# Kernel optimization log

Hardware: AMD Instinct MI355X
Metric: run time of the kernel (lower is better)

Reference implementation:

```python
import jax, jax.numpy as jnp
import numpy as np

N_NODES = 50000
N_EDGES = 800000
X_DIM = 32
E_DIM = 32
HID = 64
OUT = 32


def setup_inputs() -> dict:
    key = jax.random.key(0)
    ks = jax.random.split(key, 6)
    x = jax.random.normal(ks[0], (N_NODES, X_DIM), dtype=jnp.float32)
    edge_index = jax.random.randint(ks[1], (2, N_EDGES), 0, N_NODES, dtype=jnp.int64)
    edge_attr = jax.random.normal(ks[2], (N_EDGES, E_DIM), dtype=jnp.float32)
    in_dim = 2 * X_DIM + E_DIM  # 96
    W1 = jax.random.normal(ks[3], (in_dim, HID), dtype=jnp.float32) * (1.0 / np.sqrt(in_dim))
    b1 = jnp.zeros((HID,), dtype=jnp.float32)
    W2 = jax.random.normal(ks[4], (HID, OUT), dtype=jnp.float32) * (1.0 / np.sqrt(HID))
    b2 = jnp.zeros((OUT,), dtype=jnp.float32)
    return {"x": x, "edge_index": edge_index, "edge_attr": edge_attr,
            "W1": W1, "b1": b1, "W2": W2, "b2": b2}


def reference(x, edge_index, edge_attr, W1, b1, W2, b2):
    num_nodes = x.shape[0]
    rol, col = edge_index[0], edge_index[1]
    # gather endpoint features + edge attr -> [E, 2*x_dim + e_dim]
    e_feat = jnp.concatenate([x[rol], x[col], edge_attr], axis=-1)
    # 2-layer MLP (ReLU hidden)
    h = jax.nn.relu(e_feat @ W1 + b1)
    v = h @ W2 + b2  # [E, OUT]
    # scatter-max aggregation into destination nodes (empty segments -> -inf)
    x_cand = jax.ops.segment_max(v, col, num_segments=num_nodes)
    # elementwise max residual against trailing slice of x
    return jnp.maximum(x_cand, x[:, -v.shape[-1]:])
```

## Files before the change

kernel.cpp:

```cpp
#include <hip/hip_runtime.h>


constexpr int XD   = 32;
constexpr int HID  = 64;
constexpr int OUTD = 32;
constexpr int BM   = 128;
constexpr int ASTR = 104;
constexpr int HSTR = 72;
constexpr int BIN_SHIFT = 5;
constexpr int BINW  = 1 << BIN_SHIFT;
constexpr int BLK_E = 8192;
constexpr int EPB   = BLK_E / 256;

typedef __attribute__((ext_vector_type(8)))  short    short8;
typedef __attribute__((ext_vector_type(4)))  float    f32x4;
typedef __attribute__((ext_vector_type(4)))  float    floatx4;

static __device__ __forceinline__ unsigned f2bf(float f) {
    union { float f; unsigned u; } x; x.f = f;
    unsigned r = x.u + 0x7fff + ((x.u >> 16) & 1);
    return r >> 16;
}
static __device__ __forceinline__ unsigned encf(float f) {
    unsigned u = __float_as_uint(f);
    return (u >> 31) ? ~u : (u | 0x80000000u);
}
static __device__ __forceinline__ float decf(unsigned k) {
    return __uint_as_float((k >> 31) ? (k & 0x7fffffffu) : ~k);
}

__global__ __launch_bounds__(256) void prep_hist(
    const float* __restrict__ x, unsigned* __restrict__ xbf,
    const float* __restrict__ W1, const float* __restrict__ W2,
    unsigned* __restrict__ w1s, unsigned* __restrict__ w2s,
    const int* __restrict__ ei, unsigned* __restrict__ cnt,
    int n_edges, int nbins, int nblk, int total8)
{
    __shared__ unsigned lh[2048];
    const int t = threadIdx.x;
    const int b = blockIdx.x;

    if (b < nblk) {
        for (int i = t; i < nbins; i += 256) lh[i] = 0u;
        __syncthreads();
        const int chunk = b * BLK_E;
#pragma unroll
        for (int i = 0; i < EPB; ++i) {
            const int e = chunk + i * 256 + t;
            if (e < n_edges)
                atomicAdd(&lh[((unsigned)ei[n_edges + e]) >> BIN_SHIFT], 1u);
        }
        __syncthreads();
        for (int i = t; i < nbins; i += 256)
            cnt[(size_t)b * nbins + i] = lh[i];
        return;
    }

    const int i = (b - nblk) * 256 + t;

    if (i < total8) {
        const float4* src = reinterpret_cast<const float4*>(x) + (size_t)i * 2;
        float4 a = src[0], bb = src[1];
        uint4 o;
        o.x = f2bf(a.x)  | (f2bf(a.y)  << 16);
        o.y = f2bf(a.z)  | (f2bf(a.w)  << 16);
        o.z = f2bf(bb.x) | (f2bf(bb.y) << 16);
        o.w = f2bf(bb.z) | (f2bf(bb.w) << 16);
        reinterpret_cast<uint4*>(xbf)[i] = o;
    }

    if (i < 768) {
        const int ti = i >> 6, lane = i & 63;
        const int nt = ti / 3, ks = ti % 3;
        const int col = nt * 16 + (lane & 15);
        const int k0  = ks * 32 + ((lane >> 4) << 3);
        unsigned o[4];
#pragma unroll
        for (int p = 0; p < 4; ++p)
            o[p] = f2bf(W1[(k0 + 2 * p) * HID + col]) |
                   (f2bf(W1[(k0 + 2 * p + 1) * HID + col]) << 16);
        reinterpret_cast<uint4*>(w1s)[i] = make_uint4(o[0], o[1], o[2], o[3]);
    } else if (i < 1024) {
        const int tt = i - 768;
        const int ti = tt >> 6, lane = tt & 63;
        const int nt = ti >> 1, ks = ti & 1;
        const int col = nt * 16 + (lane & 15);
        const int k0  = ks * 32 + ((lane >> 4) << 3);
        unsigned o[4];
#pragma unroll
        for (int p = 0; p < 4; ++p)
            o[p] = f2bf(W2[(k0 + 2 * p) * OUTD + col]) |
                   (f2bf(W2[(k0 + 2 * p + 1) * OUTD + col]) << 16);
        reinterpret_cast<uint4*>(w2s)[tt] = make_uint4(o[0], o[1], o[2], o[3]);
    }
}

__global__ __launch_bounds__(128) void bin_off(
    const unsigned* __restrict__ cnt, unsigned* __restrict__ off,
    unsigned* __restrict__ totals, int nblk, int nbins)
{
    __shared__ unsigned ts[128];
    const int j = blockIdx.x;
    const int t = threadIdx.x;
    const unsigned d = (t < nblk) ? cnt[(size_t)t * nbins + j] : 0u;
    ts[t] = d;
    __syncthreads();
#pragma unroll
    for (int o = 1; o < 128; o <<= 1) {
        unsigned v = (t >= o) ? ts[t - o] : 0u;
        __syncthreads();
        ts[t] += v;
        __syncthreads();
    }
    if (t < nblk) off[(size_t)t * nbins + j] = ts[t] - d;
    if (t == 127) totals[j] = ts[127];
}

__global__ __launch_bounds__(256) void base_scan(
    const unsigned* __restrict__ totals, unsigned* __restrict__ base, int nbins)
{
    __shared__ unsigned ts[256];
    const int t = threadIdx.x;
    unsigned d[8];
    unsigned s = 0;
#pragma unroll
    for (int k = 0; k < 8; ++k) {
        const int i = t * 8 + k;
        d[k] = (i < nbins) ? totals[i] : 0u;
        s += d[k];
    }
    ts[t] = s;
    __syncthreads();
#pragma unroll
    for (int o = 1; o < 256; o <<= 1) {
        unsigned v = (t >= o) ? ts[t - o] : 0u;
        __syncthreads();
        ts[t] += v;
        __syncthreads();
    }
    unsigned run = (t == 0) ? 0u : ts[t - 1];
#pragma unroll
    for (int k = 0; k < 8; ++k) {
        const int i = t * 8 + k;
        if (i < nbins) base[i] = run;
        run += d[k];
    }
    if (t == 255) base[nbins] = run;
}

__global__ __launch_bounds__(256) void bin_write(
    const int* __restrict__ ei, const unsigned* __restrict__ off,
    const unsigned* __restrict__ base, uint2* __restrict__ rec,
    int n_edges, int nbins)
{
    __shared__ unsigned loff[2048];
    __shared__ unsigned lrank[2048];
    const int t = threadIdx.x;
    const int b = blockIdx.x;
    for (int i = t; i < nbins; i += 256) {
        loff[i]  = base[i] + off[(size_t)b * nbins + i];
        lrank[i] = 0u;
    }
    __syncthreads();
    const int chunk = b * BLK_E;
#pragma unroll
    for (int i = 0; i < EPB; ++i) {
        const int e = chunk + i * 256 + t;
        if (e < n_edges) {
            const unsigned row = (unsigned)ei[e];
            const unsigned col = (unsigned)ei[n_edges + e];
            const unsigned bin = col >> BIN_SHIFT;
            const unsigned r   = atomicAdd(&lrank[bin], 1u);
            rec[loff[bin] + r] = make_uint2((row << 16) | col, (unsigned)e);
        }
    }
}

__global__ __launch_bounds__(256) void edge_mlp_fused(
    const unsigned* __restrict__ xbf,
    const uint2*    __restrict__ rec,
    const float*    __restrict__ ea,
    const unsigned* __restrict__ w1s,
    const unsigned* __restrict__ w2s,
    const float*    __restrict__ b1,
    const float*    __restrict__ b2,
    const float*    __restrict__ x,
    const unsigned* __restrict__ base,
    float*          __restrict__ out,
    int n_edges, int n_nodes)
{
    __shared__ alignas(16) unsigned short S[BM * ASTR];
    __shared__ unsigned accK[BINW * OUTD];
    __shared__ unsigned rcsE[BM];
    __shared__ unsigned rcsR[BM];
    __shared__ unsigned rcsC[BM];

    const int t    = threadIdx.x;
    const int lane = t & 63;
    const int wave = t >> 6;
    const int bin  = blockIdx.x;
    const int n0   = bin << BIN_SHIFT;

    const unsigned sbeg = base[bin];
    const unsigned send = base[bin + 1];

    short8 w1f[12];
#pragma unroll
    for (int ti = 0; ti < 12; ++ti)
        w1f[ti] = *reinterpret_cast<const short8*>(w1s + (size_t)(ti * 64 + lane) * 4);
    short8 w2f[4];
#pragma unroll
    for (int ti = 0; ti < 4; ++ti)
        w2f[ti] = *reinterpret_cast<const short8*>(w2s + (size_t)(ti * 64 + lane) * 4);
    float bb1[4];
#pragma unroll
    for (int nt = 0; nt < 4; ++nt) bb1[nt] = b1[nt * 16 + (lane & 15)];
    float bb2[2];
#pragma unroll
    for (int nt = 0; nt < 2; ++nt) bb2[nt] = b2[nt * 16 + (lane & 15)];

#pragma unroll
    for (int k = 0; k < (BINW * OUTD) / 256; ++k) {
        const int idx = t + k * 256;
        const int g   = n0 + (idx >> 5);
        const float r = (g < n_nodes) ? x[(size_t)g * XD + (idx & 31)] : 0.0f;
        accK[idx] = encf(r);
    }

    const int ntile = (int)(send - sbeg + BM - 1) / BM;
    for (int tile = 0; tile < ntile; ++tile) {
        __syncthreads();

        if (t < BM) {
            unsigned p = sbeg + tile * BM + t;
            if (p >= send) p = send - 1;
            const uint2 q = rec[p];
            rcsE[t] = q.y; rcsR[t] = q.x >> 16; rcsC[t] = q.x & 0xffffu;
        }
        __syncthreads();

        {
            const int m    = t & 127;
            const int side = t >> 7;
            const unsigned id = side ? rcsC[m] : rcsR[m];
            const uint4* src = reinterpret_cast<const uint4*>(xbf + (size_t)id * 16);
#pragma unroll
            for (int q = 0; q < 4; ++q)
                *reinterpret_cast<uint4*>(&S[m * ASTR + side * 32 + q * 8]) = src[q];
        }
        {
#pragma unroll
            for (int i = 0; i < 4; ++i) {
                const int f = t + i * 256;
                const int m = f >> 3;
                const int c = (f & 7) * 4;
                const unsigned e = rcsE[m];
                const floatx4 d = __builtin_nontemporal_load(
                    reinterpret_cast<const floatx4*>(ea + (size_t)e * 32 + c));
                uint2 pk;
                pk.x = f2bf(d.x) | (f2bf(d.y) << 16);
                pk.y = f2bf(d.z) | (f2bf(d.w) << 16);
                *reinterpret_cast<uint2*>(&S[m * ASTR + 64 + c]) = pk;
            }
        }
        __syncthreads();

        f32x4 acc1[2][4];
#pragma unroll
        for (int mi = 0; mi < 2; ++mi)
#pragma unroll
            for (int nt = 0; nt < 4; ++nt) acc1[mi][nt] = (f32x4){0.f, 0.f, 0.f, 0.f};
#pragma unroll
        for (int ks = 0; ks < 3; ++ks) {
#pragma unroll
            for (int mi = 0; mi < 2; ++mi) {
                const int mt = wave * 2 + mi;
                short8 afrag = *reinterpret_cast<const short8*>(
                    &S[(mt * 16 + (lane & 15)) * ASTR + ks * 32 + ((lane >> 4) << 3)]);
#pragma unroll
                for (int nt = 0; nt < 4; ++nt)
                    acc1[mi][nt] = __builtin_amdgcn_mfma_f32_16x16x32_bf16(
                        afrag, w1f[nt * 3 + ks], acc1[mi][nt], 0, 0, 0);
            }
        }
        __syncthreads();

#pragma unroll
        for (int mi = 0; mi < 2; ++mi) {
            const int mt = wave * 2 + mi;
#pragma unroll
            for (int nt = 0; nt < 4; ++nt)
#pragma unroll
                for (int r = 0; r < 4; ++r) {
                    const float h = fmaxf(acc1[mi][nt][r] + bb1[nt], 0.0f);
                    S[(mt * 16 + ((lane >> 4) << 2) + r) * HSTR + nt * 16 + (lane & 15)] =
                        (unsigned short)f2bf(h);
                }
        }

        f32x4 acc2[2][2];
#pragma unroll
        for (int mi = 0; mi < 2; ++mi)
#pragma unroll
            for (int nt = 0; nt < 2; ++nt) acc2[mi][nt] = (f32x4){0.f, 0.f, 0.f, 0.f};
#pragma unroll
        for (int ks = 0; ks < 2; ++ks) {
#pragma unroll
            for (int mi = 0; mi < 2; ++mi) {
                const int mt = wave * 2 + mi;
                short8 hfrag = *reinterpret_cast<const short8*>(
                    &S[(mt * 16 + (lane & 15)) * HSTR + ks * 32 + ((lane >> 4) << 3)]);
#pragma unroll
                for (int nt = 0; nt < 2; ++nt)
                    acc2[mi][nt] = __builtin_amdgcn_mfma_f32_16x16x32_bf16(
                        hfrag, w2f[nt * 2 + ks], acc2[mi][nt], 0, 0, 0);
            }
        }

#pragma unroll
        for (int mi = 0; mi < 2; ++mi) {
            const int mt = wave * 2 + mi;
#pragma unroll
            for (int nt = 0; nt < 2; ++nt)
#pragma unroll
                for (int r = 0; r < 4; ++r) {
                    const int row = mt * 16 + ((lane >> 4) << 2) + r;
                    const float val = acc2[mi][nt][r] + bb2[nt];
                    const int ln = (int)rcsC[row] - n0;
                    atomicMax(&accK[ln * OUTD + nt * 16 + (lane & 15)], encf(val));
                }
        }
    }

    __syncthreads();
#pragma unroll
    for (int k = 0; k < (BINW * OUTD) / 256; ++k) {
        const int idx = t + k * 256;
        const int g   = n0 + (idx >> 5);
        if (g < n_nodes)
            out[(size_t)g * OUTD + (idx & 31)] = decf(accK[idx]);
    }
}

extern "C" void kernel_launch(void* const* d_in, const int* in_sizes, int n_in,
                              void* d_out, int out_size, void* d_ws, size_t ws_size,
                              hipStream_t stream)
{
    const float* x  = (const float*)d_in[0];
    const int*   ei = (const int*)  d_in[1];
    const float* ea = (const float*)d_in[2];
    const float* W1 = (const float*)d_in[3];
    const float* b1 = (const float*)d_in[4];
    const float* W2 = (const float*)d_in[5];
    const float* b2 = (const float*)d_in[6];
    float* out = (float*)d_out;

    const int n_nodes = in_sizes[0] / XD;
    const int n_edges = in_sizes[2] / 32;
    const int nbins   = (n_nodes + BINW - 1) >> BIN_SHIFT;
    const int nblk    = (n_edges + BLK_E - 1) / BLK_E;

    size_t off_b = 0;
    unsigned* cnt    = (unsigned*)((char*)d_ws + off_b); off_b += (size_t)nblk * nbins * 4;
    unsigned* offm   = (unsigned*)((char*)d_ws + off_b); off_b += (size_t)nblk * nbins * 4;
    unsigned* totals = (unsigned*)((char*)d_ws + off_b); off_b += (size_t)nbins * 4;
    unsigned* basep  = (unsigned*)((char*)d_ws + off_b); off_b += (size_t)(nbins + 1) * 4;
    off_b = (off_b + 15) & ~(size_t)15;
    uint2*    rec    = (uint2*)   ((char*)d_ws + off_b); off_b += (size_t)n_edges * 8;
    unsigned* xbf    = (unsigned*)((char*)d_ws + off_b); off_b += (size_t)n_nodes * 16 * 4;
    unsigned* w1s    = (unsigned*)((char*)d_ws + off_b); off_b += 768 * 16;
    unsigned* w2s    = (unsigned*)((char*)d_ws + off_b);

    const int total8     = n_nodes * XD / 8;
    const int prep_blk   = (max(total8, 1024) + 255) / 256;

    prep_hist<<<nblk + prep_blk, 256, 0, stream>>>(
        x, xbf, W1, W2, w1s, w2s, ei, cnt, n_edges, nbins, nblk, total8);
    bin_off<<<nbins, 128, 0, stream>>>(cnt, offm, totals, nblk, nbins);
    base_scan<<<1, 256, 0, stream>>>(totals, basep, nbins);
    bin_write<<<nblk, 256, 0, stream>>>(ei, offm, basep, rec, n_edges, nbins);
    edge_mlp_fused<<<nbins, 256, 0, stream>>>(
        xbf, rec, ea, w1s, w2s, b1, b2, x, basep, out, n_edges, n_nodes);
}
```

Measured before the change: 98.57 us.

## Prefetch next tile's edge records and edge attributes into registers

Edge record indices are now held in per-thread registers instead of shared arrays, which removes one barrier per tile. The next tile's record and its edge_attr row half are loaded into registers before the current tile's MFMA work, so global latency overlaps compute. Each thread now loads a contiguous 64-byte half of one edge's attributes instead of strided chunks. In exchange, register pressure rises from the prefetched float4s, which could lower occupancy.

Result: slower. 128.6 us (+30.5%).

```diff
diff --git a/kernel.cpp b/kernel.cpp
--- a/kernel.cpp
+++ b/kernel.cpp
@@ -191,8 +191,6 @@
 {
     __shared__ alignas(16) unsigned short S[BM * ASTR];
     __shared__ unsigned accK[BINW * OUTD];
-    __shared__ unsigned rcsE[BM];
-    __shared__ unsigned rcsR[BM];
     __shared__ unsigned rcsC[BM];
 
     const int t    = threadIdx.x;
@@ -201,6 +199,9 @@
     const int bin  = blockIdx.x;
     const int n0   = bin << BIN_SHIFT;
 
+    const int m    = t & 127;
+    const int side = t >> 7;
+
     const unsigned sbeg = base[bin];
     const unsigned send = base[bin + 1];
 
@@ -228,42 +229,60 @@
     }
 
     const int ntile = (int)(send - sbeg + BM - 1) / BM;
+
+    unsigned myE = 0, myR = 0, myC = 0;
+    floatx4  eg[4];
+
+    if (ntile > 0) {
+        unsigned p = sbeg + (unsigned)m;
+        if (p >= send) p = send - 1;
+        const uint2 q = rec[p];
+        myE = q.y; myR = q.x >> 16; myC = q.x & 0xffffu;
+        const floatx4* es = reinterpret_cast<const floatx4*>(
+            ea + (size_t)myE * 32 + side * 16);
+#pragma unroll
+        for (int k = 0; k < 4; ++k) eg[k] = __builtin_nontemporal_load(es + k);
+    }
+
     for (int tile = 0; tile < ntile; ++tile) {
-        __syncthreads();
-
-        if (t < BM) {
-            unsigned p = sbeg + tile * BM + t;
+        unsigned nE = myE, nR = myR, nC = myC;
+        if (tile + 1 < ntile) {
+            unsigned p = sbeg + (unsigned)(tile + 1) * BM + m;
             if (p >= send) p = send - 1;
             const uint2 q = rec[p];
-            rcsE[t] = q.y; rcsR[t] = q.x >> 16; rcsC[t] = q.x & 0xffffu;
-        }
+            nE = q.y; nR = q.x >> 16; nC = q.x & 0xffffu;
+        }
+
         __syncthreads();
 
         {
-            const int m    = t & 127;
-            const int side = t >> 7;
-            const unsigned id = side ? rcsC[m] : rcsR[m];
-            const uint4* src = reinterpret_cast<const uint4*>(xbf + (size_t)id * 16);
-#pragma unroll
-            for (int q = 0; q < 4; ++q)
-                *reinterpret_cast<uint4*>(&S[m * ASTR + side * 32 + q * 8]) = src[q];
-        }
-        {
-#pragma unroll
-            for (int i = 0; i < 4; ++i) {
-                const int f = t + i * 256;
-                const int m = f >> 3;
-                const int c = (f & 7) * 4;
-                const unsigned e = rcsE[m];
-                const floatx4 d = __builtin_nontemporal_load(
-                    reinterpret_cast<const floatx4*>(ea + (size_t)e * 32 + c));
+            const unsigned gid = side ? myC : myR;
+            const uint4* src = reinterpret_cast<const uint4*>(xbf + (size_t)gid * 16);
+            uint4 xg0 = src[0], xg1 = src[1], xg2 = src[2], xg3 = src[3];
+
+#pragma unroll
+            for (int k = 0; k < 4; ++k) {
                 uint2 pk;
-                pk.x = f2bf(d.x) | (f2bf(d.y) << 16);
-                pk.y = f2bf(d.z) | (f2bf(d.w) << 16);
-                *reinterpret_cast<uint2*>(&S[m * ASTR + 64 + c]) = pk;
+                pk.x = f2bf(eg[k].x) | (f2bf(eg[k].y) << 16);
+                pk.y = f2bf(eg[k].z) | (f2bf(eg[k].w) << 16);
+                *reinterpret_cast<uint2*>(&S[m * ASTR + 64 + side * 16 + k * 4]) = pk;
             }
-        }
-        __syncthreads();
+            if (side == 0) rcsC[m] = myC;
+
+            *reinterpret_cast<uint4*>(&S[m * ASTR + side * 32 +  0]) = xg0;
+            *reinterpret_cast<uint4*>(&S[m * ASTR + side * 32 +  8]) = xg1;
+            *reinterpret_cast<uint4*>(&S[m * ASTR + side * 32 + 16]) = xg2;
+            *reinterpret_cast<uint4*>(&S[m * ASTR + side * 32 + 24]) = xg3;
+        }
+        __syncthreads();
+
+        myE = nE; myR = nR; myC = nC;
+        if (tile + 1 < ntile) {
+            const floatx4* es = reinterpret_cast<const floatx4*>(
+                ea + (size_t)myE * 32 + side * 16);
+#pragma unroll
+            for (int k = 0; k < 4; ++k) eg[k] = __builtin_nontemporal_load(es + k);
+        }
 
         f32x4 acc1[2][4];
 #pragma unroll
```

## Load MFMA A-fragments directly from global memory instead of staging through LDS

Applied to the files above, without the earlier changes.

The first-layer input tile is no longer staged in shared memory. Each lane now gathers its own bf16 node-feature fragments and edge-attribute fragments from global memory straight into MFMA operand registers. This drops the LDS staging writes, the fragment reads and two block barriers per tile, and shrinks the LDS footprint, which may raise occupancy. In exchange the global loads are less coalesced: 16-byte per-lane gathers replace the cooperative row copies, the edge_attr loads lose the nontemporal hint, and each wave waits on its own loads before the MFMAs.

Result: faster. 92.21 us (-6.5%).

```diff
diff --git a/kernel.cpp b/kernel.cpp
--- a/kernel.cpp
+++ b/kernel.cpp
@@ -5,7 +5,6 @@
 constexpr int HID  = 64;
 constexpr int OUTD = 32;
 constexpr int BM   = 128;
-constexpr int ASTR = 104;
 constexpr int HSTR = 72;
 constexpr int BIN_SHIFT = 5;
 constexpr int BINW  = 1 << BIN_SHIFT;
@@ -189,7 +188,7 @@
     float*          __restrict__ out,
     int n_edges, int n_nodes)
 {
-    __shared__ alignas(16) unsigned short S[BM * ASTR];
+    __shared__ alignas(16) unsigned short Hlds[BM * HSTR];
     __shared__ unsigned accK[BINW * OUTD];
     __shared__ unsigned rcsE[BM];
     __shared__ unsigned rcsR[BM];
@@ -228,62 +227,55 @@
     }
 
     const int ntile = (int)(send - sbeg + BM - 1) / BM;
+    const int koff  = lane >> 4;
+
     for (int tile = 0; tile < ntile; ++tile) {
         __syncthreads();
 
         if (t < BM) {
-            unsigned p = sbeg + tile * BM + t;
+            unsigned p = sbeg + (unsigned)tile * BM + t;
             if (p >= send) p = send - 1;
             const uint2 q = rec[p];
             rcsE[t] = q.y; rcsR[t] = q.x >> 16; rcsC[t] = q.x & 0xffffu;
         }
         __syncthreads();
 
-        {
-            const int m    = t & 127;
-            const int side = t >> 7;
-            const unsigned id = side ? rcsC[m] : rcsR[m];
-            const uint4* src = reinterpret_cast<const uint4*>(xbf + (size_t)id * 16);
-#pragma unroll
-            for (int q = 0; q < 4; ++q)
-                *reinterpret_cast<uint4*>(&S[m * ASTR + side * 32 + q * 8]) = src[q];
-        }
-        {
-#pragma unroll
-            for (int i = 0; i < 4; ++i) {
-                const int f = t + i * 256;
-                const int m = f >> 3;
-                const int c = (f & 7) * 4;
-                const unsigned e = rcsE[m];
-                const floatx4 d = __builtin_nontemporal_load(
-                    reinterpret_cast<const floatx4*>(ea + (size_t)e * 32 + c));
-                uint2 pk;
-                pk.x = f2bf(d.x) | (f2bf(d.y) << 16);
-                pk.y = f2bf(d.z) | (f2bf(d.w) << 16);
-                *reinterpret_cast<uint2*>(&S[m * ASTR + 64 + c]) = pk;
+        f32x4 acc1[2][4];
+#pragma unroll
+        for (int mi = 0; mi < 2; ++mi)
+#pragma unroll
+            for (int nt = 0; nt < 4; ++nt) acc1[mi][nt] = (f32x4){0.f, 0.f, 0.f, 0.f};
+
+#pragma unroll
+        for (int mi = 0; mi < 2; ++mi) {
+            const int row16 = (wave * 2 + mi) * 16 + (lane & 15);
+            const unsigned idR = rcsR[row16];
+            const unsigned idC = rcsC[row16];
+            const unsigned eid = rcsE[row16];
+
+            const short8 aR = *reinterpret_cast<const short8*>(
+                xbf + (size_t)idR * 16 + koff * 4);
+            const short8 aC = *reinterpret_cast<const short8*>(
+                xbf + (size_t)idC * 16 + koff * 4);
+            const floatx4* ep = reinterpret_cast<const floatx4*>(
+                ea + (size_t)eid * 32 + koff * 8);
+            const floatx4 e0 = ep[0], e1 = ep[1];
+            union { uint4 u; short8 s; } ae;
+            ae.u.x = f2bf(e0.x) | (f2bf(e0.y) << 16);
+            ae.u.y = f2bf(e0.z) | (f2bf(e0.w) << 16);
+            ae.u.z = f2bf(e1.x) | (f2bf(e1.y) << 16);
+            ae.u.w = f2bf(e1.z) | (f2bf(e1.w) << 16);
+
+#pragma unroll
+            for (int nt = 0; nt < 4; ++nt) {
+                acc1[mi][nt] = __builtin_amdgcn_mfma_f32_16x16x32_bf16(
+                    aR, w1f[nt * 3 + 0], acc1[mi][nt], 0, 0, 0);
+                acc1[mi][nt] = __builtin_amdgcn_mfma_f32_16x16x32_bf16(
+                    aC, w1f[nt * 3 + 1], acc1[mi][nt], 0, 0, 0);
+                acc1[mi][nt] = __builtin_amdgcn_mfma_f32_16x16x32_bf16(
+                    ae.s, w1f[nt * 3 + 2], acc1[mi][nt], 0, 0, 0);
             }
         }
-        __syncthreads();
-
-        f32x4 acc1[2][4];
-#pragma unroll
-        for (int mi = 0; mi < 2; ++mi)
-#pragma unroll
-            for (int nt = 0; nt < 4; ++nt) acc1[mi][nt] = (f32x4){0.f, 0.f, 0.f, 0.f};
-#pragma unroll
-        for (int ks = 0; ks < 3; ++ks) {
-#pragma unroll
-            for (int mi = 0; mi < 2; ++mi) {
-                const int mt = wave * 2 + mi;
-                short8 afrag = *reinterpret_cast<const short8*>(
-                    &S[(mt * 16 + (lane & 15)) * ASTR + ks * 32 + ((lane >> 4) << 3)]);
-#pragma unroll
-                for (int nt = 0; nt < 4; ++nt)
-                    acc1[mi][nt] = __builtin_amdgcn_mfma_f32_16x16x32_bf16(
-                        afrag, w1f[nt * 3 + ks], acc1[mi][nt], 0, 0, 0);
-            }
-        }
-        __syncthreads();
 
 #pragma unroll
         for (int mi = 0; mi < 2; ++mi) {
@@ -293,7 +285,7 @@
 #pragma unroll
                 for (int r = 0; r < 4; ++r) {
                     const float h = fmaxf(acc1[mi][nt][r] + bb1[nt], 0.0f);
-                    S[(mt * 16 + ((lane >> 4) << 2) + r) * HSTR + nt * 16 + (lane & 15)] =
+                    Hlds[(mt * 16 + ((lane >> 4) << 2) + r) * HSTR + nt * 16 + (lane & 15)] =
                         (unsigned short)f2bf(h);
                 }
         }
@@ -309,7 +301,7 @@
             for (int mi = 0; mi < 2; ++mi) {
                 const int mt = wave * 2 + mi;
                 short8 hfrag = *reinterpret_cast<const short8*>(
-                    &S[(mt * 16 + (lane & 15)) * HSTR + ks * 32 + ((lane >> 4) << 3)]);
+                    &Hlds[(mt * 16 + (lane & 15)) * HSTR + ks * 32 + ((lane >> 4) << 3)]);
 #pragma unroll
                 for (int nt = 0; nt < 2; ++nt)
                     acc2[mi][nt] = __builtin_amdgcn_mfma_f32_16x16x32_bf16(
```
